# Optimization experiments

Measured on AMD Instinct MI355X. Metric: run time of the kernel, lower is better.

Reference implementation:

```python
import jax, jax.numpy as jnp
import numpy as np

RADIUS = [3, 3, 4, 4]
DILATION = [1, 2, 1, 2]
N_HEAD = 4
D_K = 8
SCALE = 1.0 / np.sqrt(8.0)  # module hardcodes sqrt(8)


def _patches(a, r, d):
    # a: (b, t, c, h, w) -> (b, t, c, ls2, h, w), dilated (2r+1)x(2r+1) window,
    # zero padding (invalid positions masked separately).
    b, t, c, h, w = a.shape
    p = r * d
    ap = jnp.pad(a, ((0, 0), (0, 0), (0, 0), (p, p), (p, p)))
    ls = 2 * r + 1
    sl = [ap[..., dy * d:dy * d + h, dx * d:dx * d + w]
          for dy in range(ls) for dx in range(ls)]
    return jnp.stack(sl, axis=3)


def _valid_mask(h, w, r, d):
    # (ls2, h, w) bool: True where window position is inside the image
    m = _patches(jnp.ones((1, 1, 1, h, w)), r, d)
    return m[0, 0, 0] > 0.5


def _head_attn(q, k, v, r, d):
    # q,k,v: (b, t, c, h, w); attention over all t' frames x local window
    b, t, c, h, w = q.shape
    kp = _patches(k, r, d)        # (b, t', c, p, h, w)
    vp = _patches(v, r, d)
    valid = _valid_mask(h, w, r, d)  # (p, h, w)
    e = jnp.einsum('btchw,bscphw->btsphw', q, kp) * SCALE
    e = jnp.where(valid[None, None, None], e, -jnp.inf)  # OOB -> -inf like CUDA kernel
    e = e.reshape(b, t, t * valid.shape[0], h, w)
    attn = jax.nn.softmax(e, axis=2).reshape(b, t, t, -1, h, w)
    return jnp.einsum('btsphw,bscphw->btchw', attn, vp)


def setup_inputs() -> dict:
    key = jax.random.key(0)
    kx, kq, kk, kv, ko = jax.random.split(key, 5)
    C = 32
    std = 1.0 / np.sqrt(C)
    x = jax.random.normal(kx, (2, 5, C, 64, 64), dtype=jnp.float32)
    Wq = jax.random.normal(kq, (N_HEAD * D_K, C), dtype=jnp.float32) * std
    Wk = jax.random.normal(kk, (N_HEAD * D_K, C), dtype=jnp.float32) * std
    Wv = jax.random.normal(kv, (N_HEAD * D_K, C), dtype=jnp.float32) * std
    Wo = jax.random.normal(ko, (C, C), dtype=jnp.float32) * std
    return {"x": x, "Wq": Wq, "Wk": Wk, "Wv": Wv, "Wo": Wo}


def reference(x, Wq, Wk, Wv, Wo):
    # 1x1x1 Conv3d == per-pixel channel matmul
    q = jnp.einsum('btchw,kc->btkhw', x, Wq)
    k = jnp.einsum('btchw,kc->btkhw', x, Wk)
    v = jnp.einsum('btchw,kc->btkhw', x, Wv)
    outs = []
    for i in range(N_HEAD):
        s = slice(i * D_K, (i + 1) * D_K)
        outs.append(_head_attn(q[:, :, s], k[:, :, s], v[:, :, s],
                               RADIUS[i], DILATION[i]))
    out = jnp.concatenate(outs, axis=2)
    out = jnp.einsum('btchw,kc->btkhw', out, Wo)
    return out + x
```

## Files before the change

### kernel.cpp

```cpp
#include <hip/hip_runtime.h>
#include <stdint.h>

#define NT 5
#define NC 32
#define NH 4
#define HW 4096
#define NPIX 40960
#define QS 0.51006972789f
#define EBIAS 12.0f
#define NINF (-__builtin_inff())

typedef _Float16 half_t;
typedef half_t h2 __attribute__((ext_vector_type(2)));

static __device__ __forceinline__ h2 as_h2(uint32_t u) {
  union { uint32_t u; h2 h; } c; c.u = u; return c.h;
}
static __device__ __forceinline__ uint32_t pack_h2(float a, float b) {
  union { h2 h; uint32_t u; } c;
  c.h.x = (half_t)a; c.h.y = (half_t)b;
  return c.u;
}

#if __has_builtin(__builtin_amdgcn_exp2f)
#define EXP2(x) __builtin_amdgcn_exp2f(x)
#else
#define EXP2(x) exp2f(x)
#endif

static __device__ __forceinline__ float dot8i(const uint4& a, const uint4& b, float c) {
#if __has_builtin(__builtin_amdgcn_fdot2)
  c = __builtin_amdgcn_fdot2(as_h2(a.x), as_h2(b.x), c, false);
  c = __builtin_amdgcn_fdot2(as_h2(a.y), as_h2(b.y), c, false);
  c = __builtin_amdgcn_fdot2(as_h2(a.z), as_h2(b.z), c, false);
  c = __builtin_amdgcn_fdot2(as_h2(a.w), as_h2(b.w), c, false);
  return c;
#else
  const h2 a0 = as_h2(a.x), a1 = as_h2(a.y), a2 = as_h2(a.z), a3 = as_h2(a.w);
  const h2 b0 = as_h2(b.x), b1 = as_h2(b.y), b2 = as_h2(b.z), b3 = as_h2(b.w);
  c = fmaf((float)a0.x, (float)b0.x, c);
  c = fmaf((float)a0.y, (float)b0.y, c);
  c = fmaf((float)a1.x, (float)b1.x, c);
  c = fmaf((float)a1.y, (float)b1.y, c);
  c = fmaf((float)a2.x, (float)b2.x, c);
  c = fmaf((float)a2.y, (float)b2.y, c);
  c = fmaf((float)a3.x, (float)b3.x, c);
  c = fmaf((float)a3.y, (float)b3.y, c);
  return c;
#endif
}

__global__ __launch_bounds__(256) void qkv_kernel(
    const float* __restrict__ x,
    const float* __restrict__ Wq, const float* __restrict__ Wk,
    const float* __restrict__ Wv,
    uint2* __restrict__ qf, uint2* __restrict__ kf, uint2* __restrict__ vf)
{
  const int p   = blockIdx.x * 256 + threadIdx.x;
  const int by  = blockIdx.y;
  const int h   = by >> 1;
  const int jg  = by & 1;
  const int bt  = p >> 12;
  const int pix = p & 4095;

  const float* xp = x + (size_t)bt * (NC * HW) + pix;
  float xc[NC];
  #pragma unroll
  for (int c = 0; c < NC; ++c) xc[c] = xp[(size_t)c * HW];

  float qv[4], kv4[4], vv4[4];
  #pragma unroll
  for (int j = 0; j < 4; ++j) {
    const int o = h * 8 + jg * 4 + j;
    float aq = 0.f, ak = 0.f, av = 0.f;
    #pragma unroll
    for (int c = 0; c < NC; ++c) {
      const float xv = xc[c];
      aq = fmaf(xv, Wq[o * NC + c], aq);
      ak = fmaf(xv, Wk[o * NC + c], ak);
      av = fmaf(xv, Wv[o * NC + c], av);
    }
    qv[j] = aq * QS; kv4[j] = ak; vv4[j] = av;
  }
  const size_t base = (((size_t)bt * NH + h) * HW + pix) * 2 + jg;
  uint2 qq, kk, vv;
  qq.x = pack_h2(qv[0], qv[1]);  qq.y = pack_h2(qv[2], qv[3]);
  kk.x = pack_h2(kv4[0], kv4[1]); kk.y = pack_h2(kv4[2], kv4[3]);
  vv.x = pack_h2(vv4[0], vv4[1]); vv.y = pack_h2(vv4[2], vv4[3]);
  qf[base] = qq;
  kf[base] = kk;
  vf[base] = vv;
}

template <int R, int D>
static __device__ __forceinline__ void attn_body(
    int b, int t, int h, int s, int yb,
    const uint4* __restrict__ qf, const uint4* __restrict__ kf,
    const uint4* __restrict__ vf,
    uint4* __restrict__ pa, float* __restrict__ pl,
    uint4* __restrict__ k_lds, uint4* __restrict__ v_lds)
{
  constexpr int LS    = 2 * R + 1;
  constexpr int NROWS = 4 + 2 * R;
  const int tid  = threadIdx.x;
  const int w    = tid >> 6;
  const int lane = tid & 63;

  const int y0 = (D == 1) ? (yb * 4) : ((yb & 1) + 8 * (yb >> 1));

  const uint4* kg = kf + (size_t)((b * NT + s) * NH + h) * HW;
  const uint4* vg = vf + (size_t)((b * NT + s) * NH + h) * HW;
  for (int idx = tid; idx < NROWS * 64; idx += 128) {
    const int r  = idx >> 6, xs = idx & 63;
    int ys = y0 + (r - R) * D;
    ys = ys < 0 ? 0 : (ys > 63 ? 63 : ys);
    const int pos = (D == 1) ? xs : ((xs & 1) * 32 + (xs >> 1));
    k_lds[r * 64 + pos] = kg[ys * 64 + xs];
    v_lds[r * 64 + pos] = vg[ys * 64 + xs];
  }
  __syncthreads();

  const int xp = lane >> 5;
  const int cb = (D == 1) ? lane : (lane & 31);
  const int x  = (D == 1) ? lane : (2 * (lane & 31) + xp);
  const int yA = y0 + 2 * w * D;
  const int yB = yA + D;
  const int pixA = yA * 64 + x, pixB = yB * 64 + x;

  const uint4* qp = qf + (size_t)((b * NT + t) * NH + h) * HW;
  const uint4 qA = qp[pixA];
  const uint4 qB = qp[pixB];

  float lA = 0.f, lB = 0.f;
  h2 aA[4], aB[4];
  const h2 z2 = { (half_t)0.f, (half_t)0.f };
  #pragma unroll
  for (int i = 0; i < 4; ++i) { aA[i] = z2; aB[i] = z2; }

  #pragma unroll 2
  for (int u = 0; u <= LS; ++u) {
    const int ykey = y0 + (2 * w + u - R) * D;
    const bool oky = (unsigned)ykey < 64u;
    const bool okA = (u < LS) && oky;
    const bool okB = (u > 0)  && oky;
    if (!(okA || okB)) continue;
    const float biA = okA ? -EBIAS : NINF;
    const float biB = okB ? -EBIAS : NINF;
    const uint4* kr = k_lds + (2 * w + u) * 64;
    const uint4* vr = v_lds + (2 * w + u) * 64;
    #pragma unroll
    for (int dx = -R; dx <= R; ++dx) {
      const int  cx  = cb + dx;
      const bool okx = (unsigned)cx < (D == 1 ? 64u : 32u);
      const int  cc  = okx ? cx : 0;
      const int  pos = (D == 1) ? cc : (xp * 32 + cc);
      const uint4 kk = kr[pos];
      const uint4 vv = vr[pos];
      const h2 w0 = as_h2(vv.x), w1 = as_h2(vv.y), w2 = as_h2(vv.z), w3 = as_h2(vv.w);
      const float eo = okx ? 0.f : NINF;
      const float pA = EXP2(dot8i(qA, kk, biA + eo));
      const float pB = EXP2(dot8i(qB, kk, biB + eo));
      lA += pA; lB += pB;
      const half_t pAh = (half_t)pA, pBh = (half_t)pB;
      const h2 pA2 = { pAh, pAh }, pB2 = { pBh, pBh };
      aA[0] += pA2 * w0; aA[1] += pA2 * w1; aA[2] += pA2 * w2; aA[3] += pA2 * w3;
      aB[0] += pB2 * w0; aB[1] += pB2 * w1; aB[2] += pB2 * w2; aB[3] += pB2 * w3;
    }
  }

  const size_t plane = (size_t)(s * NH + h) * NPIX + (size_t)(b * NT + t) * HW;
  union { h2 hh[4]; uint4 u; } cA, cB;
  #pragma unroll
  for (int i = 0; i < 4; ++i) { cA.hh[i] = aA[i]; cB.hh[i] = aB[i]; }
  pa[plane + pixA] = cA.u;
  pa[plane + pixB] = cB.u;
  pl[plane + pixA] = lA;
  pl[plane + pixB] = lB;
}

__global__ __launch_bounds__(128, 4) void attn_kernel(
    const uint4* __restrict__ qf, const uint4* __restrict__ kf,
    const uint4* __restrict__ vf, uint4* __restrict__ pa, float* __restrict__ pl)
{
  __shared__ uint4 k_lds[12 * 64];
  __shared__ uint4 v_lds[12 * 64];
  const int bid = blockIdx.x;
  const int h   = bid & 3;
  int r = bid >> 2;
  const int yb = r & 15; r >>= 4;
  const int s  = r % 5;
  const int bt = r / 5;
  const int t = bt % NT, b = bt / NT;
  if      (h == 0) attn_body<3, 1>(b, t, 0, s, yb, qf, kf, vf, pa, pl, k_lds, v_lds);
  else if (h == 1) attn_body<3, 2>(b, t, 1, s, yb, qf, kf, vf, pa, pl, k_lds, v_lds);
  else if (h == 2) attn_body<4, 1>(b, t, 2, s, yb, qf, kf, vf, pa, pl, k_lds, v_lds);
  else             attn_body<4, 2>(b, t, 3, s, yb, qf, kf, vf, pa, pl, k_lds, v_lds);
}

__global__ __launch_bounds__(256) void proj_kernel(
    const uint4* __restrict__ pa, const float* __restrict__ pl,
    const float* __restrict__ x, const float* __restrict__ Wo,
    float* __restrict__ out)
{
  const int p   = blockIdx.x * 256 + threadIdx.x;
  const int og  = blockIdx.y;
  const int bt  = p >> 12;
  const int pix = p & 4095;

  float oc[32];
  #pragma unroll
  for (int h = 0; h < NH; ++h) {
    float a[8], l = 0.f;
    #pragma unroll
    for (int i = 0; i < 8; ++i) a[i] = 0.f;
    #pragma unroll
    for (int s = 0; s < NT; ++s) {
      const size_t plane = (size_t)(s * NH + h) * NPIX + p;
      const uint4 v = pa[plane];
      l += pl[plane];
      const h2 v0 = as_h2(v.x), v1 = as_h2(v.y), v2 = as_h2(v.z), v3 = as_h2(v.w);
      a[0] += (float)v0.x; a[1] += (float)v0.y;
      a[2] += (float)v1.x; a[3] += (float)v1.y;
      a[4] += (float)v2.x; a[5] += (float)v2.y;
      a[6] += (float)v3.x; a[7] += (float)v3.y;
    }
    const float inv = 1.0f / l;
    #pragma unroll
    for (int i = 0; i < 8; ++i) oc[h * 8 + i] = a[i] * inv;
  }

  const float* xpt = x + (size_t)bt * (NC * HW) + pix;
  float* yp = out + (size_t)bt * (NC * HW) + pix;
  #pragma unroll
  for (int oo = 0; oo < 8; ++oo) {
    const int o = og * 8 + oo;
    float acc = xpt[(size_t)o * HW];
    #pragma unroll
    for (int c = 0; c < NC; ++c)
      acc = fmaf(oc[c], Wo[o * NC + c], acc);
    yp[(size_t)o * HW] = acc;
  }
}

extern "C" void kernel_launch(void* const* d_in, const int* in_sizes, int n_in,
                              void* d_out, int out_size, void* d_ws, size_t ws_size,
                              hipStream_t stream)
{
  const float* x  = (const float*)d_in[0];
  const float* Wq = (const float*)d_in[1];
  const float* Wk = (const float*)d_in[2];
  const float* Wv = (const float*)d_in[3];
  const float* Wo = (const float*)d_in[4];

  char* ws = (char*)d_ws;
  uint2* qf = (uint2*)ws;
  uint2* kf = (uint2*)(ws + 2621440);
  uint2* vf = (uint2*)(ws + 2 * 2621440);
  uint4* pa = (uint4*)(ws + 3 * 2621440);
  float* pl = (float*)(ws + 3 * 2621440 + 13107200);

  qkv_kernel<<<dim3(160, 8), 256, 0, stream>>>(x, Wq, Wk, Wv, qf, kf, vf);
  attn_kernel<<<3200, 128, 0, stream>>>((const uint4*)qf, (const uint4*)kf,
                                        (const uint4*)vf, pa, pl);
  proj_kernel<<<dim3(160, 4), 256, 0, stream>>>(pa, pl, x, Wo, (float*)d_out);
}
```

Before: 120.3 us.

## Process all query frames per attention block to reuse staged K/V tiles

Each attention block now loops over all five query frames, holding five q vectors and five sets of accumulators per pixel. This reuses each K/V row loaded into LDS across all frames instead of reloading it per frame, and cuts the grid from 3200 to 640 blocks. Blocks are ordered so the larger-radius heads are scheduled first. The projection kernel now computes 4 output channels per block with twice as many blocks. The cost is much higher register pressure (the occupancy hint in launch bounds is dropped) and fewer blocks, which may lower occupancy on the GPU.

After: 132.1 us. 9.8% more time.

```diff
diff --git a/kernel.cpp b/kernel.cpp
--- a/kernel.cpp
+++ b/kernel.cpp
@@ -94,7 +94,7 @@
 
 template <int R, int D>
 static __device__ __forceinline__ void attn_body(
-    int b, int t, int h, int s, int yb,
+    int b, int h, int s, int yb,
     const uint4* __restrict__ qf, const uint4* __restrict__ kf,
     const uint4* __restrict__ vf,
     uint4* __restrict__ pa, float* __restrict__ pl,
@@ -127,17 +127,25 @@
   const int yB = yA + D;
   const int pixA = yA * 64 + x, pixB = yB * 64 + x;
 
-  const uint4* qp = qf + (size_t)((b * NT + t) * NH + h) * HW;
-  const uint4 qA = qp[pixA];
-  const uint4 qB = qp[pixB];
-
-  float lA = 0.f, lB = 0.f;
-  h2 aA[4], aB[4];
+  uint4 qA[NT], qB[NT];
+  #pragma unroll
+  for (int t = 0; t < NT; ++t) {
+    const uint4* qp = qf + (size_t)((b * NT + t) * NH + h) * HW;
+    qA[t] = qp[pixA];
+    qB[t] = qp[pixB];
+  }
+
+  float lA[NT], lB[NT];
+  h2 aA[NT][4], aB[NT][4];
   const h2 z2 = { (half_t)0.f, (half_t)0.f };
   #pragma unroll
-  for (int i = 0; i < 4; ++i) { aA[i] = z2; aB[i] = z2; }
-
-  #pragma unroll 2
+  for (int t = 0; t < NT; ++t) {
+    lA[t] = 0.f; lB[t] = 0.f;
+    #pragma unroll
+    for (int i = 0; i < 4; ++i) { aA[t][i] = z2; aB[t][i] = z2; }
+  }
+
+  #pragma unroll 1
   for (int u = 0; u <= LS; ++u) {
     const int ykey = y0 + (2 * w + u - R) * D;
     const bool oky = (unsigned)ykey < 64u;
@@ -149,52 +157,62 @@
     const uint4* kr = k_lds + (2 * w + u) * 64;
     const uint4* vr = v_lds + (2 * w + u) * 64;
     #pragma unroll
-    for (int dx = -R; dx <= R; ++dx) {
-      const int  cx  = cb + dx;
+    for (int i = 0; i < LS; ++i) {
+      const int  cx  = cb + i - R;
       const bool okx = (unsigned)cx < (D == 1 ? 64u : 32u);
       const int  cc  = okx ? cx : 0;
       const int  pos = (D == 1) ? cc : (xp * 32 + cc);
       const uint4 kk = kr[pos];
       const uint4 vv = vr[pos];
+      const float eo  = okx ? 0.f : NINF;
+      const float ciA = biA + eo;
+      const float ciB = biB + eo;
       const h2 w0 = as_h2(vv.x), w1 = as_h2(vv.y), w2 = as_h2(vv.z), w3 = as_h2(vv.w);
-      const float eo = okx ? 0.f : NINF;
-      const float pA = EXP2(dot8i(qA, kk, biA + eo));
-      const float pB = EXP2(dot8i(qB, kk, biB + eo));
-      lA += pA; lB += pB;
-      const half_t pAh = (half_t)pA, pBh = (half_t)pB;
-      const h2 pA2 = { pAh, pAh }, pB2 = { pBh, pBh };
-      aA[0] += pA2 * w0; aA[1] += pA2 * w1; aA[2] += pA2 * w2; aA[3] += pA2 * w3;
-      aB[0] += pB2 * w0; aB[1] += pB2 * w1; aB[2] += pB2 * w2; aB[3] += pB2 * w3;
+      #pragma unroll
+      for (int t = 0; t < NT; ++t) {
+        const float pA = EXP2(dot8i(qA[t], kk, ciA));
+        const float pB = EXP2(dot8i(qB[t], kk, ciB));
+        lA[t] += pA; lB[t] += pB;
+        const half_t pAh = (half_t)pA, pBh = (half_t)pB;
+        const h2 pA2 = { pAh, pAh }, pB2 = { pBh, pBh };
+        aA[t][0] += pA2 * w0; aA[t][1] += pA2 * w1;
+        aA[t][2] += pA2 * w2; aA[t][3] += pA2 * w3;
+        aB[t][0] += pB2 * w0; aB[t][1] += pB2 * w1;
+        aB[t][2] += pB2 * w2; aB[t][3] += pB2 * w3;
+      }
     }
   }
 
-  const size_t plane = (size_t)(s * NH + h) * NPIX + (size_t)(b * NT + t) * HW;
-  union { h2 hh[4]; uint4 u; } cA, cB;
-  #pragma unroll
-  for (int i = 0; i < 4; ++i) { cA.hh[i] = aA[i]; cB.hh[i] = aB[i]; }
-  pa[plane + pixA] = cA.u;
-  pa[plane + pixB] = cB.u;
-  pl[plane + pixA] = lA;
-  pl[plane + pixB] = lB;
-}
-
-__global__ __launch_bounds__(128, 4) void attn_kernel(
+  #pragma unroll
+  for (int t = 0; t < NT; ++t) {
+    const size_t plane = (size_t)(s * NH + h) * NPIX + (size_t)(b * NT + t) * HW;
+    union { h2 hh[4]; uint4 u; } cA, cB;
+    #pragma unroll
+    for (int i = 0; i < 4; ++i) { cA.hh[i] = aA[t][i]; cB.hh[i] = aB[t][i]; }
+    pa[plane + pixA] = cA.u;
+    pa[plane + pixB] = cB.u;
+    pl[plane + pixA] = lA[t];
+    pl[plane + pixB] = lB[t];
+  }
+}
+
+__global__ __launch_bounds__(128) void attn_kernel(
     const uint4* __restrict__ qf, const uint4* __restrict__ kf,
     const uint4* __restrict__ vf, uint4* __restrict__ pa, float* __restrict__ pl)
 {
   __shared__ uint4 k_lds[12 * 64];
   __shared__ uint4 v_lds[12 * 64];
   const int bid = blockIdx.x;
-  const int h   = bid & 3;
-  int r = bid >> 2;
-  const int yb = r & 15; r >>= 4;
-  const int s  = r % 5;
-  const int bt = r / 5;
-  const int t = bt % NT, b = bt / NT;
-  if      (h == 0) attn_body<3, 1>(b, t, 0, s, yb, qf, kf, vf, pa, pl, k_lds, v_lds);
-  else if (h == 1) attn_body<3, 2>(b, t, 1, s, yb, qf, kf, vf, pa, pl, k_lds, v_lds);
-  else if (h == 2) attn_body<4, 1>(b, t, 2, s, yb, qf, kf, vf, pa, pl, k_lds, v_lds);
-  else             attn_body<4, 2>(b, t, 3, s, yb, qf, kf, vf, pa, pl, k_lds, v_lds);
+  int h, rest;
+  if (bid < 320) { h = 2 + (bid & 1); rest = bid >> 1; }
+  else           { h = ((bid - 320) & 1); rest = (bid - 320) >> 1; }
+  const int yb = rest & 15; rest >>= 4;
+  const int s  = rest % 5;
+  const int b  = rest / 5;
+  if      (h == 0) attn_body<3, 1>(b, 0, s, yb, qf, kf, vf, pa, pl, k_lds, v_lds);
+  else if (h == 1) attn_body<3, 2>(b, 1, s, yb, qf, kf, vf, pa, pl, k_lds, v_lds);
+  else if (h == 2) attn_body<4, 1>(b, 2, s, yb, qf, kf, vf, pa, pl, k_lds, v_lds);
+  else             attn_body<4, 2>(b, 3, s, yb, qf, kf, vf, pa, pl, k_lds, v_lds);
 }
 
 __global__ __launch_bounds__(256) void proj_kernel(
@@ -232,8 +250,8 @@
   const float* xpt = x + (size_t)bt * (NC * HW) + pix;
   float* yp = out + (size_t)bt * (NC * HW) + pix;
   #pragma unroll
-  for (int oo = 0; oo < 8; ++oo) {
-    const int o = og * 8 + oo;
+  for (int oo = 0; oo < 4; ++oo) {
+    const int o = og * 4 + oo;
     float acc = xpt[(size_t)o * HW];
     #pragma unroll
     for (int c = 0; c < NC; ++c)
@@ -260,7 +278,7 @@
   float* pl = (float*)(ws + 3 * 2621440 + 13107200);
 
   qkv_kernel<<<dim3(160, 8), 256, 0, stream>>>(x, Wq, Wk, Wv, qf, kf, vf);
-  attn_kernel<<<3200, 128, 0, stream>>>((const uint4*)qf, (const uint4*)kf,
-                                        (const uint4*)vf, pa, pl);
-  proj_kernel<<<dim3(160, 4), 256, 0, stream>>>(pa, pl, x, Wo, (float*)d_out);
-}
+  attn_kernel<<<640, 128, 0, stream>>>((const uint4*)qf, (const uint4*)kf,
+                                       (const uint4*)vf, pa, pl);
+  proj_kernel<<<dim3(160, 8), 256, 0, stream>>>(pa, pl, x, Wo, (float*)d_out);
+}
```
